# Optimization experiments

Hardware: AMD Instinct MI355X
Metric: run time of the kernel (lower is better)

The kernel has to match this reference:

```python
import jax, jax.numpy as jnp
import numpy as np
import math

B, N, M, C, H = 4, 2048, 2048, 512, 4
D_V = C // H          # 128, used for scale and value head dim
D_QK = 2 * C // H     # 256, q/k head dim due to seq-axis split of the 2*dim qkv output
SCALE = D_V ** -0.5
EPS = 1e-12           # F.normalize eps


def _l2norm(t):
    n = jnp.linalg.norm(t, axis=-1, keepdims=True)
    return t / jnp.maximum(n, EPS)


def setup_inputs() -> dict:
    key = jax.random.key(0)
    k1, k2, k3, k4 = jax.random.split(key, 4)
    x = jax.random.normal(k1, (B, N, C), dtype=jnp.float32)
    context = jax.random.normal(k2, (B, M, C), dtype=jnp.float32)
    W_qkv = jax.random.normal(k3, (2 * C, C), dtype=jnp.float32) * 0.02  # torch Linear weight [out,in]
    W_proj = jax.random.normal(k4, (C, C), dtype=jnp.float32) * 0.02
    radius = jnp.ones((H,), dtype=jnp.float32) * math.sqrt(D_V)
    return {"x": x, "context": context, "W_qkv": W_qkv, "W_proj": W_proj, "radius": radius}


def reference(x, context, W_qkv, W_proj, radius):
    # qkv(cat([x, context], dim=1)) then split along sequence: q from x rows, k from context rows
    q = jnp.einsum('bnc,oc->bno', x, W_qkv)        # [B,N,2C]
    k = jnp.einsum('bmc,oc->bmo', context, W_qkv)  # [B,M,2C]
    q = q.reshape(B, N, H, D_QK).transpose(0, 2, 1, 3)       # [B,H,N,256]
    k = k.reshape(B, M, H, D_QK).transpose(0, 2, 1, 3)       # [B,H,M,256]
    v = context.reshape(B, M, H, D_V).transpose(0, 2, 1, 3)  # [B,H,M,128]
    r = radius[None, :, None, None]
    q = _l2norm(q) * r
    k = _l2norm(k) * r
    attn = jnp.einsum('bhnd,bhmd->bhnm', q, k) * SCALE
    attn = jax.nn.softmax(attn, axis=-1)
    out = jnp.einsum('bhnm,bhmd->bhnd', attn, v)
    out = out.transpose(0, 2, 1, 3).reshape(B, N, C)
    return jnp.einsum('bnc,oc->bno', out, W_proj)
```

## Files before the change

kernel.cpp:

```cpp
#include <hip/hip_runtime.h>
#include <hip/hip_bf16.h>
#include <stdint.h>

#define SCALE_F 0.08838834764831845f

typedef __attribute__((ext_vector_type(8))) short short8;
typedef __attribute__((ext_vector_type(4))) float f32x4;

__device__ __forceinline__ void g2l16(const void* g, void* l) {
  __builtin_amdgcn_global_load_lds(
      (const __attribute__((address_space(1))) void*)g,
      (__attribute__((address_space(3))) void*)l, 16, 0, 0);
}

__global__ __launch_bounds__(256) void convert_all(
    const float* __restrict__ x, const float* __restrict__ ctx,
    const float* __restrict__ wqkv, const float* __restrict__ wproj,
    __hip_bfloat16* __restrict__ ab, __hip_bfloat16* __restrict__ wb,
    __hip_bfloat16* __restrict__ wpb)
{
  size_t qi = (size_t)blockIdx.x * 256 + threadIdx.x;
  const float* src; __hip_bfloat16* dst; size_t off;
  if (qi < 1048576)      { src = x;     dst = ab;           off = qi; }
  else if (qi < 2097152) { src = ctx;   dst = ab + 4194304; off = qi - 1048576; }
  else if (qi < 2228224) { src = wqkv;  dst = wb;           off = qi - 2097152; }
  else                   { src = wproj; dst = wpb;          off = qi - 2228224; }
  float4 v = ((const float4*)src)[off];
  union { __hip_bfloat16 h4[4]; uint2 u; } o;
  o.h4[0] = __float2bfloat16(v.x); o.h4[1] = __float2bfloat16(v.y);
  o.h4[2] = __float2bfloat16(v.z); o.h4[3] = __float2bfloat16(v.w);
  ((uint2*)dst)[off] = o.u;
}

__global__ __launch_bounds__(256) void transpose_v(
    const float* __restrict__ ctx, __hip_bfloat16* __restrict__ vt)
{
  __shared__ float tile[128][33];
  const int bid = blockIdx.x;
  const int mt = bid & 63;
  const int bh = bid >> 6;
  const int h = bh & 3, b = bh >> 2;
  const int tid = threadIdx.x;
  for (int i = 0; i < 16; ++i) {
    int idx = i * 256 + tid;
    int mm = idx >> 7, d = idx & 127;
    tile[d][mm] = ctx[((size_t)b * 2048 + mt * 32 + mm) * 512 + h * 128 + d];
  }
  __syncthreads();
  for (int i = 0; i < 16; ++i) {
    int idx = i * 256 + tid;
    int d = idx >> 5, mm = idx & 31;
    vt[((size_t)bh * 128 + d) * 2048 + mt * 32 + mm] = __float2bfloat16(tile[d][mm]);
  }
}

__global__ __launch_bounds__(256) void gemm_nt(
    const __hip_bfloat16* __restrict__ A, const __hip_bfloat16* __restrict__ B,
    float* __restrict__ C, int O, int K, int tiles_o)
{
  __shared__ __hip_bfloat16 sA[128 * 32];
  __shared__ __hip_bfloat16 sB[128 * 32];
  const int tid = threadIdx.x;
  const int wave = tid >> 6, lane = tid & 63;
  const int ln = lane & 15, q = lane >> 4;
  const int br = (blockIdx.x / tiles_o) * 128;
  const int bo = (blockIdx.x % tiles_o) * 128;
  const int wr = (wave >> 1) * 64, wc = (wave & 1) * 64;
  const __hip_bfloat16* Ab = A + (size_t)br * K;
  const __hip_bfloat16* Bb = B + (size_t)bo * K;
  const int row0 = tid >> 2, p0 = tid & 3;
  f32x4 acc[4][4] = {};
  for (int k0 = 0; k0 < K; k0 += 32) {
    for (int i = 0; i < 2; ++i) {
      int row = i * 64 + row0;
      g2l16(Ab + (size_t)row * K + k0 + p0 * 8, (char*)sA + (i * 256 + tid) * 16);
      g2l16(Bb + (size_t)row * K + k0 + p0 * 8, (char*)sB + (i * 256 + tid) * 16);
    }
    __syncthreads();
    short8 af[4], bfr[4];
    for (int mi = 0; mi < 4; ++mi)
      af[mi] = *(const short8*)(sA + (wr + mi * 16 + ln) * 32 + q * 8);
    for (int ni = 0; ni < 4; ++ni)
      bfr[ni] = *(const short8*)(sB + (wc + ni * 16 + ln) * 32 + q * 8);
    for (int mi = 0; mi < 4; ++mi)
      for (int ni = 0; ni < 4; ++ni)
        acc[mi][ni] = __builtin_amdgcn_mfma_f32_16x16x32_bf16(af[mi], bfr[ni], acc[mi][ni], 0, 0, 0);
    __syncthreads();
  }
  for (int mi = 0; mi < 4; ++mi)
    for (int ni = 0; ni < 4; ++ni) {
      int rg = br + wr + mi * 16 + q * 4;
      int cg = bo + wc + ni * 16 + ln;
      for (int r = 0; r < 4; ++r)
        C[(size_t)(rg + r) * O + cg] = acc[mi][ni][r];
    }
}

__global__ __launch_bounds__(256) void normalize_qk(
    const float* __restrict__ proj, const float* __restrict__ radius,
    __hip_bfloat16* __restrict__ qn, __hip_bfloat16* __restrict__ kn)
{
  const int r = blockIdx.x;
  const int h = threadIdx.x >> 6, lane = threadIdx.x & 63;
  float4 v = *(const float4*)(proj + (size_t)r * 1024 + h * 256 + lane * 4);
  float ss = v.x * v.x + v.y * v.y + v.z * v.z + v.w * v.w;
  for (int off = 1; off < 64; off <<= 1) ss += __shfl_xor(ss, off);
  float nrm = fmaxf(sqrtf(ss), 1e-12f);
  const bool isq = r < 8192;
  const int rr = isq ? r : r - 8192;
  const float rad = radius[h];
  const float sc = (isq ? rad * rad * SCALE_F : 1.0f) / nrm;
  __hip_bfloat16* dst = (isq ? qn : kn) +
      ((size_t)((rr >> 11) * 4 + h) * 2048 + (rr & 2047)) * 256 + lane * 4;
  union { __hip_bfloat16 h4[4]; uint2 u; } o;
  o.h4[0] = __float2bfloat16(v.x * sc);
  o.h4[1] = __float2bfloat16(v.y * sc);
  o.h4[2] = __float2bfloat16(v.z * sc);
  o.h4[3] = __float2bfloat16(v.w * sc);
  *(uint2*)dst = o.u;
}

__global__ __launch_bounds__(256) void attn(
    const __hip_bfloat16* __restrict__ qn,
    const __hip_bfloat16* __restrict__ kn,
    const __hip_bfloat16* __restrict__ vt,
    __hip_bfloat16* __restrict__ ob)
{
  __shared__ __hip_bfloat16 sK[8 * 64 * 32];
  __shared__ __hip_bfloat16 sV[128 * 72];
  __shared__ __hip_bfloat16 sP[4][16 * 72];
  const int tid = threadIdx.x, wave = tid >> 6, lane = tid & 63;
  const int ln = lane & 15, q = lane >> 4;
  const int nt = blockIdx.x & 31, bh = blockIdx.x >> 5;
  const __hip_bfloat16* Q = qn + ((size_t)bh * 2048 + nt * 64 + wave * 16) * 256;
  const __hip_bfloat16* Kp = kn + (size_t)bh * 2048 * 256;
  const __hip_bfloat16* Vp = vt + (size_t)bh * 128 * 2048;
  short8 qf[8];
  for (int kk = 0; kk < 8; ++kk)
    qf[kk] = *(const short8*)(Q + ln * 256 + kk * 32 + q * 8);
  f32x4 oacc[8] = {};
  float denom[4] = {0.f, 0.f, 0.f, 0.f};
  __hip_bfloat16* sPw = sP[wave];
  const int krow = tid >> 2, kp = tid & 3;
  for (int m0 = 0; m0 < 2048; m0 += 64) {
    for (int i = 0; i < 8; ++i)
      g2l16(Kp + (size_t)(m0 + krow) * 256 + i * 32 + kp * 8,
            (char*)sK + i * 4096 + tid * 16);
    for (int i = 0; i < 4; ++i) {
      int flat = i * 256 + tid;
      int d = flat >> 3, p = flat & 7;
      short8 t = *(const short8*)(Vp + (size_t)d * 2048 + m0 + p * 8);
      *(short8*)((char*)sV + d * 144 + p * 16) = t;
    }
    __syncthreads();
    f32x4 s[4];
    for (int ni = 0; ni < 4; ++ni) {
      f32x4 a = {};
      for (int kk = 0; kk < 8; ++kk) {
        short8 kf = *(const short8*)((char*)sK + kk * 4096 + (ni * 16 + ln) * 64 + q * 16);
        a = __builtin_amdgcn_mfma_f32_16x16x32_bf16(qf[kk], kf, a, 0, 0, 0);
      }
      s[ni] = a;
    }
    float psum[4] = {0.f, 0.f, 0.f, 0.f};
    for (int ni = 0; ni < 4; ++ni)
      for (int r = 0; r < 4; ++r) {
        float e = __expf(s[ni][r]);
        psum[r] += e;
        sPw[(q * 4 + r) * 72 + ni * 16 + ln] = __float2bfloat16(e);
      }
    for (int off = 1; off < 16; off <<= 1)
      for (int r = 0; r < 4; ++r) psum[r] += __shfl_xor(psum[r], off);
    for (int r = 0; r < 4; ++r) denom[r] += psum[r];
    asm volatile("s_waitcnt lgkmcnt(0)" ::: "memory");
    for (int kc = 0; kc < 2; ++kc) {
      short8 pf = *(const short8*)((char*)sPw + ln * 144 + kc * 64 + q * 16);
      for (int vi = 0; vi < 8; ++vi) {
        short8 vf = *(const short8*)((char*)sV + (vi * 16 + ln) * 144 + kc * 64 + q * 16);
        oacc[vi] = __builtin_amdgcn_mfma_f32_16x16x32_bf16(pf, vf, oacc[vi], 0, 0, 0);
      }
    }
    __syncthreads();
  }
  const int b = bh >> 2, h = bh & 3;
  const int nrow = nt * 64 + wave * 16 + q * 4;
  for (int vi = 0; vi < 8; ++vi)
    for (int r = 0; r < 4; ++r) {
      float o = oacc[vi][r] / denom[r];
      ob[((size_t)b * 2048 + nrow + r) * 512 + h * 128 + vi * 16 + ln] = __float2bfloat16(o);
    }
}

extern "C" void kernel_launch(void* const* d_in, const int* in_sizes, int n_in,
                              void* d_out, int out_size, void* d_ws, size_t ws_size,
                              hipStream_t stream) {
  const float* x      = (const float*)d_in[0];
  const float* ctx    = (const float*)d_in[1];
  const float* wqkv   = (const float*)d_in[2];
  const float* wproj  = (const float*)d_in[3];
  const float* radius = (const float*)d_in[4];
  char* ws = (char*)d_ws;
  __hip_bfloat16* ab  = (__hip_bfloat16*)(ws);
  __hip_bfloat16* wb  = (__hip_bfloat16*)(ws + 16777216);
  __hip_bfloat16* wpb = (__hip_bfloat16*)(ws + 17825792);
  float*          proj= (float*)(ws + 18350080);
  __hip_bfloat16* qn  = (__hip_bfloat16*)(ws + 85458944);
  __hip_bfloat16* kn  = (__hip_bfloat16*)(ws + 102236160);
  __hip_bfloat16* vt  = (__hip_bfloat16*)(ws + 119013376);
  __hip_bfloat16* ob  = (__hip_bfloat16*)(ws + 127401984);
  float* out = (float*)d_out;

  convert_all<<<8960, 256, 0, stream>>>(x, ctx, wqkv, wproj, ab, wb, wpb);
  transpose_v<<<1024, 256, 0, stream>>>(ctx, vt);
  gemm_nt<<<1024, 256, 0, stream>>>(ab, wb, proj, 1024, 512, 8);
  normalize_qk<<<16384, 256, 0, stream>>>(proj, radius, qn, kn);
  attn<<<512, 256, 0, stream>>>(qn, kn, vt, ob);
  gemm_nt<<<256, 256, 0, stream>>>(ob, wpb, out, 512, 512, 4);
}
```

Baseline: 258.5 us.

## Rework attention with 32x32 MFMA, double-buffered swizzled K/V tiles, larger query tiles

```diff
diff --git a/kernel.cpp b/kernel.cpp
--- a/kernel.cpp
+++ b/kernel.cpp
@@ -6,6 +6,7 @@
 
 typedef __attribute__((ext_vector_type(8))) short short8;
 typedef __attribute__((ext_vector_type(4))) float f32x4;
+typedef __attribute__((ext_vector_type(16))) float f32x16;
 
 __device__ __forceinline__ void g2l16(const void* g, void* l) {
   __builtin_amdgcn_global_load_lds(
@@ -120,74 +121,96 @@
   *(uint2*)dst = o.u;
 }
 
-__global__ __launch_bounds__(256) void attn(
+__global__ __launch_bounds__(256, 1) void attn(
     const __hip_bfloat16* __restrict__ qn,
     const __hip_bfloat16* __restrict__ kn,
     const __hip_bfloat16* __restrict__ vt,
     __hip_bfloat16* __restrict__ ob)
 {
-  __shared__ __hip_bfloat16 sK[8 * 64 * 32];
-  __shared__ __hip_bfloat16 sV[128 * 72];
-  __shared__ __hip_bfloat16 sP[4][16 * 72];
+  __shared__ __hip_bfloat16 sK[2][32 * 256];
+  __shared__ __hip_bfloat16 sV[2][128 * 32];
+  __shared__ __hip_bfloat16 sP[4][32 * 40];
   const int tid = threadIdx.x, wave = tid >> 6, lane = tid & 63;
-  const int ln = lane & 15, q = lane >> 4;
-  const int nt = blockIdx.x & 31, bh = blockIdx.x >> 5;
-  const __hip_bfloat16* Q = qn + ((size_t)bh * 2048 + nt * 64 + wave * 16) * 256;
+  const int m32 = lane & 31, hi = lane >> 5;
+  const int nt = blockIdx.x & 15, bh = blockIdx.x >> 4;
+  const __hip_bfloat16* Q = qn + ((size_t)bh * 2048 + nt * 128 + wave * 32) * 256;
   const __hip_bfloat16* Kp = kn + (size_t)bh * 2048 * 256;
   const __hip_bfloat16* Vp = vt + (size_t)bh * 128 * 2048;
-  short8 qf[8];
-  for (int kk = 0; kk < 8; ++kk)
-    qf[kk] = *(const short8*)(Q + ln * 256 + kk * 32 + q * 8);
-  f32x4 oacc[8] = {};
-  float denom[4] = {0.f, 0.f, 0.f, 0.f};
+
+  short8 qf[16];
+  for (int kk = 0; kk < 16; ++kk)
+    qf[kk] = *(const short8*)(Q + m32 * 256 + kk * 16 + hi * 8);
+
+  f32x16 oacc[4];
+  float denom[16];
+  for (int i = 0; i < 4; ++i)
+    for (int j = 0; j < 16; ++j) oacc[i][j] = 0.f;
+  for (int j = 0; j < 16; ++j) denom[j] = 0.f;
   __hip_bfloat16* sPw = sP[wave];
-  const int krow = tid >> 2, kp = tid & 3;
-  for (int m0 = 0; m0 < 2048; m0 += 64) {
-    for (int i = 0; i < 8; ++i)
-      g2l16(Kp + (size_t)(m0 + krow) * 256 + i * 32 + kp * 8,
-            (char*)sK + i * 4096 + tid * 16);
-    for (int i = 0; i < 4; ++i) {
-      int flat = i * 256 + tid;
-      int d = flat >> 3, p = flat & 7;
-      short8 t = *(const short8*)(Vp + (size_t)d * 2048 + m0 + p * 8);
-      *(short8*)((char*)sV + d * 144 + p * 16) = t;
+
+  for (int i = 0; i < 4; ++i) {
+    int D = i * 256 + tid, row = D >> 5, cc = D & 31;
+    g2l16(Kp + (size_t)row * 256 + ((cc ^ (row & 7)) << 3), (char*)sK[0] + D * 16);
+  }
+  for (int i = 0; i < 2; ++i) {
+    int D = i * 256 + tid, rd = D >> 2, cc = D & 3;
+    g2l16(Vp + (size_t)rd * 2048 + ((cc ^ ((rd >> 1) & 3)) << 3), (char*)sV[0] + D * 16);
+  }
+  __syncthreads();
+
+  for (int it = 0; it < 64; ++it) {
+    const int cur = it & 1, nxt = cur ^ 1;
+    if (it + 1 < 64) {
+      const int m1 = (it + 1) * 32;
+      for (int i = 0; i < 4; ++i) {
+        int D = i * 256 + tid, row = D >> 5, cc = D & 31;
+        g2l16(Kp + (size_t)(m1 + row) * 256 + ((cc ^ (row & 7)) << 3),
+              (char*)sK[nxt] + D * 16);
+      }
+      for (int i = 0; i < 2; ++i) {
+        int D = i * 256 + tid, rd = D >> 2, cc = D & 3;
+        g2l16(Vp + (size_t)rd * 2048 + m1 + ((cc ^ ((rd >> 1) & 3)) << 3),
+              (char*)sV[nxt] + D * 16);
+      }
+    }
+    const __hip_bfloat16* sKc = sK[cur];
+    f32x16 s;
+    for (int j = 0; j < 16; ++j) s[j] = 0.f;
+    for (int kk = 0; kk < 16; ++kk) {
+      int c = kk * 2 + hi;
+      short8 kf = *(const short8*)(sKc + m32 * 256 + ((c ^ (m32 & 7)) << 3));
+      s = __builtin_amdgcn_mfma_f32_32x32x16_bf16(qf[kk], kf, s, 0, 0, 0);
+    }
+    for (int reg = 0; reg < 16; ++reg) {
+      float e = __expf(s[reg]);
+      denom[reg] += e;
+      int row = (reg & 3) + 8 * (reg >> 2) + 4 * hi;
+      sPw[row * 40 + m32] = __float2bfloat16(e);
+    }
+    asm volatile("s_waitcnt lgkmcnt(0)" ::: "memory");
+    const __hip_bfloat16* sVc = sV[cur];
+    for (int kc = 0; kc < 2; ++kc) {
+      short8 pf = *(const short8*)(sPw + m32 * 40 + kc * 16 + hi * 8);
+      for (int vi = 0; vi < 4; ++vi) {
+        int rd = vi * 32 + m32;
+        int c = kc * 2 + hi;
+        short8 vf = *(const short8*)(sVc + rd * 32 + ((c ^ ((rd >> 1) & 3)) << 3));
+        oacc[vi] = __builtin_amdgcn_mfma_f32_32x32x16_bf16(pf, vf, oacc[vi], 0, 0, 0);
+      }
     }
     __syncthreads();
-    f32x4 s[4];
-    for (int ni = 0; ni < 4; ++ni) {
-      f32x4 a = {};
-      for (int kk = 0; kk < 8; ++kk) {
-        short8 kf = *(const short8*)((char*)sK + kk * 4096 + (ni * 16 + ln) * 64 + q * 16);
-        a = __builtin_amdgcn_mfma_f32_16x16x32_bf16(qf[kk], kf, a, 0, 0, 0);
-      }
-      s[ni] = a;
-    }
-    float psum[4] = {0.f, 0.f, 0.f, 0.f};
-    for (int ni = 0; ni < 4; ++ni)
-      for (int r = 0; r < 4; ++r) {
-        float e = __expf(s[ni][r]);
-        psum[r] += e;
-        sPw[(q * 4 + r) * 72 + ni * 16 + ln] = __float2bfloat16(e);
-      }
-    for (int off = 1; off < 16; off <<= 1)
-      for (int r = 0; r < 4; ++r) psum[r] += __shfl_xor(psum[r], off);
-    for (int r = 0; r < 4; ++r) denom[r] += psum[r];
-    asm volatile("s_waitcnt lgkmcnt(0)" ::: "memory");
-    for (int kc = 0; kc < 2; ++kc) {
-      short8 pf = *(const short8*)((char*)sPw + ln * 144 + kc * 64 + q * 16);
-      for (int vi = 0; vi < 8; ++vi) {
-        short8 vf = *(const short8*)((char*)sV + (vi * 16 + ln) * 144 + kc * 64 + q * 16);
-        oacc[vi] = __builtin_amdgcn_mfma_f32_16x16x32_bf16(pf, vf, oacc[vi], 0, 0, 0);
-      }
-    }
-    __syncthreads();
-  }
+  }
+
+  for (int reg = 0; reg < 16; ++reg)
+    for (int off = 1; off < 32; off <<= 1)
+      denom[reg] += __shfl_xor(denom[reg], off);
+
   const int b = bh >> 2, h = bh & 3;
-  const int nrow = nt * 64 + wave * 16 + q * 4;
-  for (int vi = 0; vi < 8; ++vi)
-    for (int r = 0; r < 4; ++r) {
-      float o = oacc[vi][r] / denom[r];
-      ob[((size_t)b * 2048 + nrow + r) * 512 + h * 128 + vi * 16 + ln] = __float2bfloat16(o);
+  for (int vi = 0; vi < 4; ++vi)
+    for (int reg = 0; reg < 16; ++reg) {
+      int row = nt * 128 + wave * 32 + (reg & 3) + 8 * (reg >> 2) + 4 * hi;
+      float o = oacc[vi][reg] / denom[reg];
+      ob[((size_t)b * 2048 + row) * 512 + h * 128 + vi * 32 + m32] = __float2bfloat16(o);
     }
 }
 
@@ -214,6 +237,6 @@
   transpose_v<<<1024, 256, 0, stream>>>(ctx, vt);
   gemm_nt<<<1024, 256, 0, stream>>>(ab, wb, proj, 1024, 512, 8);
   normalize_qk<<<16384, 256, 0, stream>>>(proj, radius, qn, kn);
-  attn<<<512, 256, 0, stream>>>(qn, kn, vt, ob);
+  attn<<<256, 256, 0, stream>>>(qn, kn, vt, ob);
   gemm_nt<<<256, 256, 0, stream>>>(ob, wpb, out, 512, 512, 4);
 }
```

Result: faster. 253.3 us (-2.0%).
